# Kernel tuning notes

Measured on AMD Instinct MI355X. Metric: run time of the kernel, lower is better.

The kernel has to match this reference:

```python
import jax, jax.numpy as jnp
import numpy as np


def conv1x1(x, w, b):
    # x: [B,C,H,W], w: [O,C], b: [O]
    return jnp.einsum('bchw,oc->bohw', x, w) + b[None, :, None, None]


def setup_inputs() -> dict:
    key = jax.random.key(0)
    ks = jax.random.split(key, 16)
    B, C, H, W = 2, 64, 64, 64
    Cq = C // 8  # scale=8
    def mkw(k, o, i):
        return jax.random.normal(k, (o, i), jnp.float32) * 0.05
    return {
        'x': jax.random.normal(ks[0], (B, C, H, W), jnp.float32),
        'y': jax.random.normal(ks[1], (B, C, H, W), jnp.float32),
        'z': jax.random.normal(ks[2], (B, C, H, W), jnp.float32),
        # PAM params
        'pam_wq': mkw(ks[3], Cq, C), 'pam_bq': jnp.zeros((Cq,), jnp.float32),
        'pam_wk1': mkw(ks[4], Cq, C), 'pam_bk1': jnp.zeros((Cq,), jnp.float32),
        'pam_wk2': mkw(ks[5], Cq, C), 'pam_bk2': jnp.zeros((Cq,), jnp.float32),
        'pam_wk3': mkw(ks[6], Cq, C), 'pam_bk3': jnp.zeros((Cq,), jnp.float32),
        'pam_wv': mkw(ks[7], C, C), 'pam_bv': jnp.zeros((C,), jnp.float32),
        'pam_wl': mkw(ks[8], C, C), 'pam_bl': jnp.zeros((C,), jnp.float32),
        'pam_gamma': jnp.full((1,), 0.5, jnp.float32),
        # CAM params
        'cam_wl': mkw(ks[9], C, C), 'cam_bl': jnp.zeros((C,), jnp.float32),
        'cam_gamma': jnp.full((1,), 0.5, jnp.float32),
    }


def _pam(x, y, z, wq, bq, wk1, bk1, wk2, bk2, wk3, bk3, wv, bv, wl, bl, gamma):
    B, C, H, W = x.shape
    N = H * W
    Q = conv1x1(x, wq, bq).reshape(B, -1, N)   # [B, C/8, N]
    K1 = conv1x1(x, wk1, bk1).reshape(B, -1, N)
    K2 = conv1x1(y, wk2, bk2).reshape(B, -1, N)
    K3 = conv1x1(z, wk3, bk3).reshape(B, -1, N)
    V = conv1x1(x, wv, bv).reshape(B, C, N)    # [B, C, N]
    def branch(K):
        # energy[b,n,m] = sum_c Q[b,c,n] K[b,c,m]; softmax over last dim
        A = jax.nn.softmax(jnp.einsum('bcn,bcm->bnm', Q, K), axis=-1)
        # out[b,c,n] = sum_m A_as_mn[b,m,n] V[b,c,m] (einsum relabels axes as in torch code)
        return jnp.einsum('bmn,bcm->bcn', A, V)
    out = branch(K1) + branch(K2) + branch(K3)
    out = conv1x1(out.reshape(B, C, H, W), wl, bl)
    return x + gamma * out


def _cam(x, y, z, wl, bl, gamma):
    B, C, H, W = x.shape
    N = H * W
    q = x.reshape(B, C, N)
    def branch(k):
        e = jnp.einsum('bcn,bdn->bcd', q, k.reshape(B, C, N))  # [B,C,C]
        e = jnp.max(e, axis=-1, keepdims=True) - e             # max-subtraction trick
        A = jax.nn.softmax(e, axis=-1)
        return jnp.einsum('bcd,bdn->bcn', A, q)
    out = branch(x) + branch(y) + branch(z)
    out = conv1x1(out.reshape(B, C, H, W), wl, bl)
    return gamma * out + x


def reference(x, y, z, pam_wq, pam_bq, pam_wk1, pam_bk1, pam_wk2, pam_bk2,
              pam_wk3, pam_bk3, pam_wv, pam_bv, pam_wl, pam_bl, pam_gamma,
              cam_wl, cam_bl, cam_gamma):
    p = _pam(x, y, z, pam_wq, pam_bq, pam_wk1, pam_bk1, pam_wk2, pam_bk2,
             pam_wk3, pam_bk3, pam_wv, pam_bv, pam_wl, pam_bl, pam_gamma)
    c = _cam(x, y, z, cam_wl, cam_bl, cam_gamma)
    return p + c
```

## Files before the change

kernel.cpp:

```cpp
#include <hip/hip_runtime.h>
#include <hip/hip_bf16.h>


typedef __attribute__((ext_vector_type(8))) short bf16x8;
typedef __attribute__((ext_vector_type(4))) float f32x4;

#define MFMA16(a, b, c) __builtin_amdgcn_mfma_f32_16x16x32_bf16(a, b, c, 0, 0, 0)
#define EX2(x) __builtin_amdgcn_exp2f(x)
#define LOG2E 1.4426950408889634f

__device__ __forceinline__ float bf2f(ushort u) {
  union { unsigned int i; float f; } v; v.i = ((unsigned int)u) << 16; return v.f;
}
__device__ __forceinline__ ushort f2bf(float f) {
  union { float f; unsigned int i; } v; v.f = f;
  unsigned int r = v.i + 0x7FFFu + ((v.i >> 16) & 1u);
  return (ushort)(r >> 16);
}
__device__ __forceinline__ float loadf(const void* p, size_t i, int isbf) {
  return isbf ? bf2f(((const ushort*)p)[i]) : ((const float*)p)[i];
}
__device__ __forceinline__ bf16x8 load8(const void* p, size_t i, int isbf) {
  if (isbf) return *(const bf16x8*)((const ushort*)p + i);
  const float* f = (const float*)p + i;
  bf16x8 r;
#pragma unroll
  for (int j = 0; j < 8; ++j) r[j] = (short)f2bf(f[j]);
  return r;
}
__device__ __forceinline__ void loadf8(const void* p, size_t i, int isbf, float* o) {
  if (isbf) {
    bf16x8 v = *(const bf16x8*)((const ushort*)p + i);
#pragma unroll
    for (int j = 0; j < 8; ++j) o[j] = bf2f((ushort)v[j]);
  } else {
    const float* f = (const float*)p + i;
#pragma unroll
    for (int j = 0; j < 8; ++j) o[j] = f[j];
  }
}
__device__ __forceinline__ int detect_isbf(const unsigned int* xw, int* sflag) {
  int t = threadIdx.x;
  if (t < 64) {
    unsigned int w1 = xw[t], w2 = xw[64 + t];
    unsigned int e1 = (w1 >> 7) & 0xFFu, e2 = (w2 >> 7) & 0xFFu;
    unsigned long long b1 = __ballot(e1 >= 120u && e1 <= 133u);
    unsigned long long b2 = __ballot(e2 >= 120u && e2 <= 133u);
    if (t == 0) *sflag = (__popcll(b1) + __popcll(b2) > 64) ? 1 : 0;
  }
  __syncthreads();
  return *sflag;
}

__global__ __launch_bounds__(256) void k_prep_all(
    const void* __restrict__ x, const void* __restrict__ y, const void* __restrict__ z,
    const void* __restrict__ wq, const void* __restrict__ bq,
    const void* __restrict__ wk1, const void* __restrict__ bk1,
    const void* __restrict__ wk2, const void* __restrict__ bk2,
    const void* __restrict__ wk3, const void* __restrict__ bk3,
    const void* __restrict__ wv, const void* __restrict__ bv,
    ushort* __restrict__ QT, ushort* __restrict__ KT, ushort* __restrict__ V,
    float* __restrict__ e_part)
{
  __shared__ float wsh[4][8][64];
  __shared__ int sflag;
  int isbf = detect_isbf((const unsigned int*)x, &sflag);
  int blk = blockIdx.x, t = threadIdx.x;

  if (blk < 128) {
    for (int i = t; i < 2048; i += 256) {
      int mat = i >> 9, rem = i & 511;
      const void* src = (mat == 0) ? wq : (mat == 1) ? wk1 : (mat == 2) ? wk2 : wk3;
      wsh[mat][rem >> 6][rem & 63] = loadf(src, rem, isbf);
    }
    __syncthreads();
    int gid = blk * 256 + t;
    int qid = gid & 3;
    int n = (gid >> 2) & 4095;
    int b = gid >> 14;
    int c0 = qid * 16;
    float a[4][8];
#pragma unroll
    for (int m = 0; m < 4; ++m)
#pragma unroll
      for (int o = 0; o < 8; ++o) a[m][o] = 0.f;
    size_t base = (size_t)b * 262144 + n;
    for (int cc = 0; cc < 16; ++cc) {
      int c = c0 + cc;
      float xv = loadf(x, base + (size_t)c * 4096, isbf);
      float yv = loadf(y, base + (size_t)c * 4096, isbf);
      float zv = loadf(z, base + (size_t)c * 4096, isbf);
#pragma unroll
      for (int o = 0; o < 8; ++o) {
        a[0][o] += wsh[0][o][c] * xv;
        a[1][o] += wsh[1][o][c] * xv;
        a[2][o] += wsh[2][o][c] * yv;
        a[3][o] += wsh[3][o][c] * zv;
      }
    }
#pragma unroll
    for (int m = 0; m < 4; ++m)
#pragma unroll
      for (int o = 0; o < 8; ++o) {
        float v = a[m][o];
        v += __shfl_xor(v, 1, 64);
        v += __shfl_xor(v, 2, 64);
        a[m][o] = v;
      }
    int br = qid - 1;
    const void* bias = (qid == 0) ? bq : (qid == 1) ? bk1 : (qid == 2) ? bk2 : bk3;
    ushort* dst = (qid == 0) ? QT + (size_t)(b * 4096 + n) * 32
                             : KT + (size_t)((b * 3 + br) * 4096 + n) * 32;
    ushort row[32];
#pragma unroll
    for (int o = 0; o < 8; ++o) {
      float v = a[qid][o] + loadf(bias, o, isbf);
      row[o] = f2bf(qid == 0 ? LOG2E * v : v);
    }
#pragma unroll
    for (int o = 8; o < 32; ++o)
      row[o] = (qid > 0 && (o == 8 + 2 * br || o == 9 + 2 * br)) ? (ushort)0x3F80 : (ushort)0;
#pragma unroll
    for (int o = 0; o < 32; o += 2)
      *(unsigned int*)(dst + o) = (unsigned int)row[o] | ((unsigned int)row[o + 1] << 16);
  } else if (blk < 384) {
    int tid2 = (blk - 128) * 256 + t;
    int b = tid2 >> 15, c = (tid2 >> 9) & 63, m0 = (tid2 & 511) * 8;
    float acc[8], xv[8];
    float bb = loadf(bv, c, isbf);
#pragma unroll
    for (int j = 0; j < 8; ++j) acc[j] = bb;
    size_t xb = (size_t)b * 262144 + m0;
    for (int d = 0; d < 64; ++d) {
      float w = loadf(wv, c * 64 + d, isbf);
      loadf8(x, xb + (size_t)d * 4096, isbf, xv);
#pragma unroll
      for (int j = 0; j < 8; ++j) acc[j] += w * xv[j];
    }
    bf16x8 o8;
#pragma unroll
    for (int j = 0; j < 8; ++j) o8[j] = (short)f2bf(acc[j]);
    *(bf16x8*)(V + (size_t)(b * 64 + c) * 4096 + m0) = o8;
  } else {
    int r2 = blk - 384;
    int ns = r2 & 15, r = r2 >> 4;
    int k = r % 3, b = r / 3;
    const void* A = x;
    const void* B = (k == 0) ? x : (k == 1) ? y : z;
    size_t boff = (size_t)b * 262144;
    int w = t >> 6, l = t & 63;
    int l15 = l & 15, lh = l >> 4;
    int cbase = 16 * w;
    f32x4 acc[4];
#pragma unroll
    for (int i = 0; i < 4; ++i) acc[i] = (f32x4){0.f, 0.f, 0.f, 0.f};
    int n0 = ns * 256;
    for (int step = 0; step < 8; ++step) {
      int nb = n0 + step * 32;
      bf16x8 af = load8(A, boff + (size_t)(cbase + l15) * 4096 + nb + lh * 8, isbf);
#pragma unroll
      for (int dt = 0; dt < 4; ++dt) {
        bf16x8 bfr = load8(B, boff + (size_t)(dt * 16 + l15) * 4096 + nb + lh * 8, isbf);
        acc[dt] = MFMA16(af, bfr, acc[dt]);
      }
    }
    float* out = e_part + (size_t)(((b * 3 + k) * 16 + ns) * 64) * 64;
#pragma unroll
    for (int dt = 0; dt < 4; ++dt)
#pragma unroll
      for (int rr = 0; rr < 4; ++rr) {
        int c = cbase + lh * 4 + rr, d = dt * 16 + l15;
        out[c * 64 + d] = acc[dt][rr];
      }
  }
}

__global__ __launch_bounds__(256) void k_pass1(
    const ushort* __restrict__ QT, const ushort* __restrict__ KT,
    const float* __restrict__ e_part, float* __restrict__ S_part, float* __restrict__ e_red)
{
  int blk = blockIdx.x, t = threadIdx.x;
  if (blk < 1536) {
    int sl = blk & 3, mc = (blk >> 2) & 63, r3 = blk >> 8;
    int br = r3 % 3, b = r3 / 3;
    int w = t >> 6, l = t & 63;
    int l15 = l & 15, lh = l >> 4;
    int mbase = mc * 64 + w * 16;
    bf16x8 qf = *(const bf16x8*)(QT + (size_t)(b * 4096 + mbase + l15) * 32 + lh * 8);
    const ushort* Kb = KT + (size_t)((b * 3 + br) * 4096) * 32;
    float s = 0.f;
    int ns0 = sl * 64;
#pragma unroll 4
    for (int ns = ns0; ns < ns0 + 64; ++ns) {
      bf16x8 kf = *(const bf16x8*)(Kb + (size_t)(ns * 16 + l15) * 32 + lh * 8);
      f32x4 d = MFMA16(kf, qf, ((f32x4){0.f, 0.f, 0.f, 0.f}));
      s += EX2(d[0]) + EX2(d[1]) + EX2(d[2]) + EX2(d[3]);
    }
    s += __shfl_xor(s, 16, 64);
    s += __shfl_xor(s, 32, 64);
    if (l < 16) S_part[sl * 24576 + (b * 3 + br) * 4096 + mbase + l] = s;
  } else {
    int i = (blk - 1536) * 256 + t;
    const float* p = e_part + (size_t)(i >> 12) * 65536 + (i & 4095);
    float s = 0.f;
#pragma unroll
    for (int ks = 0; ks < 16; ++ks) s += p[ks * 4096];
    e_red[i] = s;
  }
}

__global__ __launch_bounds__(256) void k_mid(
    const float* __restrict__ S_part, ushort* __restrict__ QT,
    const float* __restrict__ e_red, const void* __restrict__ x,
    const void* __restrict__ cam_wl, const void* __restrict__ cam_bl, const void* __restrict__ cam_gamma,
    const void* __restrict__ pam_wl, const void* __restrict__ pam_bl, const void* __restrict__ pam_gamma,
    ushort* __restrict__ Wfull, float* __restrict__ biasv)
{
  int blk = blockIdx.x, t = threadIdx.x;
  if (blk < 96) {
    int i = blk * 256 + t;
    float S = S_part[i] + S_part[24576 + i] + S_part[49152 + i] + S_part[73728 + i];
    float nL = -__builtin_amdgcn_logf(S);
    int m = i & 4095, b3br = i >> 12;
    int br = b3br % 3, b = b3br / 3;
    ushort c = f2bf(nL);
    ushort r = f2bf(nL - bf2f(c));
    ushort* qrow = QT + (size_t)(b * 4096 + m) * 32;
    qrow[8 + 2 * br] = c;
    qrow[9 + 2 * br] = r;
  } else {
    __shared__ float Atot[64][65];
    __shared__ float erow[64][65];
    __shared__ int sflag;
    int isbf = detect_isbf((const unsigned int*)x, &sflag);
    int b = blk - 96;
    int r = t >> 2, q = t & 3;
#pragma unroll
    for (int j = 0; j < 16; ++j) Atot[r][q * 16 + j] = 0.f;
    for (int k = 0; k < 3; ++k) {
      const float* ep = e_red + (size_t)(b * 3 + k) * 4096;
      for (int i = t; i < 4096; i += 256) erow[i >> 6][i & 63] = ep[i];
      __syncthreads();
      float ev[16];
      float mn = 1e30f;
#pragma unroll
      for (int j = 0; j < 16; ++j) { ev[j] = erow[r][q * 16 + j]; mn = fminf(mn, ev[j]); }
      mn = fminf(mn, __shfl_xor(mn, 1, 64));
      mn = fminf(mn, __shfl_xor(mn, 2, 64));
      float s = 0.f;
#pragma unroll
      for (int j = 0; j < 16; ++j) { ev[j] = __expf(mn - ev[j]); s += ev[j]; }
      s += __shfl_xor(s, 1, 64);
      s += __shfl_xor(s, 2, 64);
      float inv = 1.0f / s;
#pragma unroll
      for (int j = 0; j < 16; ++j) Atot[r][q * 16 + j] += ev[j] * inv;
      __syncthreads();
    }
    float gc = loadf(cam_gamma, 0, isbf), gp = loadf(pam_gamma, 0, isbf);
    int c = t >> 2, d0 = (t & 3) * 16;
    float a[16];
#pragma unroll
    for (int i = 0; i < 16; ++i) a[i] = 0.f;
    for (int e = 0; e < 64; ++e) {
      float wv = loadf(cam_wl, c * 64 + e, isbf);
#pragma unroll
      for (int i = 0; i < 16; ++i) a[i] += wv * Atot[e][d0 + i];
    }
#pragma unroll
    for (int i = 0; i < 16; ++i) {
      int d = d0 + i;
      Wfull[(size_t)(b * 64 + c) * 128 + d]      = f2bf(gc * a[i]);
      Wfull[(size_t)(b * 64 + c) * 128 + 64 + d] = f2bf(gp * loadf(pam_wl, c * 64 + d, isbf));
    }
    if (b == 0 && t < 64) biasv[t] = gp * loadf(pam_bl, t, isbf) + gc * loadf(cam_bl, t, isbf);
  }
}

__global__ __launch_bounds__(256) void k_pam_out(
    const ushort* __restrict__ QT, const ushort* __restrict__ KT, const ushort* __restrict__ V,
    ushort* __restrict__ pam_part)
{
  __shared__ ushort plds[2][32 * 64];
  int blk = blockIdx.x;
  int ms = blk & 3, nt = (blk >> 2) & 127, b = blk >> 9;
  int w = threadIdx.x >> 6, l = threadIdx.x & 63;
  int l15 = l & 15, lh = l >> 4;
  int n0 = nt * 32;

  bf16x8 kf[3][2];
#pragma unroll
  for (int br = 0; br < 3; ++br)
#pragma unroll
    for (int n16 = 0; n16 < 2; ++n16)
      kf[br][n16] = *(const bf16x8*)(KT + (size_t)((b * 3 + br) * 4096 + n0 + n16 * 16 + l15) * 32 + lh * 8);

  f32x4 acc[2];
  acc[0] = (f32x4){0.f, 0.f, 0.f, 0.f};
  acc[1] = (f32x4){0.f, 0.f, 0.f, 0.f};
  const ushort* Vb = V + (size_t)(b * 64 + 16 * w + l15) * 4096;

  for (int ch = 0; ch < 16; ++ch) {
    int mch = ms * 1024 + ch * 64;
    char* buf = (char*)plds[ch & 1];
    bf16x8 qf = *(const bf16x8*)(QT + (size_t)(b * 4096 + mch + 16 * w + l15) * 32 + lh * 8);
#pragma unroll
    for (int n16 = 0; n16 < 2; ++n16) {
      f32x4 d0 = MFMA16(qf, kf[0][n16], ((f32x4){0.f, 0.f, 0.f, 0.f}));
      f32x4 d1 = MFMA16(qf, kf[1][n16], ((f32x4){0.f, 0.f, 0.f, 0.f}));
      f32x4 d2 = MFMA16(qf, kf[2][n16], ((f32x4){0.f, 0.f, 0.f, 0.f}));
      float p0 = EX2(d0[0]) + EX2(d1[0]) + EX2(d2[0]);
      float p1 = EX2(d0[1]) + EX2(d1[1]) + EX2(d2[1]);
      float p2 = EX2(d0[2]) + EX2(d1[2]) + EX2(d2[2]);
      float p3 = EX2(d0[3]) + EX2(d1[3]) + EX2(d2[3]);
      unsigned int u0, u1;
      asm("v_cvt_pk_bf16_f32 %0, %1, %2" : "=v"(u0) : "v"(p0), "v"(p1));
      asm("v_cvt_pk_bf16_f32 %0, %1, %2" : "=v"(u1) : "v"(p2), "v"(p3));
      int nl = n16 * 16 + l15;
      int byte = (nl * 128 + (16 * w + lh * 4) * 2) ^ ((nl & 7) << 4);
      *(uint2*)(buf + byte) = make_uint2(u0, u1);
    }
    __syncthreads();
#pragma unroll
    for (int ks = 0; ks < 2; ++ks) {
      bf16x8 vf = *(const bf16x8*)(Vb + mch + ks * 32 + lh * 8);
#pragma unroll
      for (int n16 = 0; n16 < 2; ++n16) {
        int nl = n16 * 16 + l15;
        int byte = (nl * 128 + (ks * 32 + lh * 8) * 2) ^ ((nl & 7) << 4);
        bf16x8 pf = *(const bf16x8*)((const char*)buf + byte);
        acc[n16] = MFMA16(vf, pf, acc[n16]);
      }
    }
  }
  ushort* outp = pam_part + (size_t)((b * 4 + ms) * 64) * 4096;
#pragma unroll
  for (int n16 = 0; n16 < 2; ++n16)
#pragma unroll
    for (int r = 0; r < 4; ++r) {
      int c = 16 * w + lh * 4 + r, n = n0 + n16 * 16 + l15;
      outp[(size_t)c * 4096 + n] = f2bf(acc[n16][r]);
    }
}

__global__ __launch_bounds__(256) void k_final(
    const void* __restrict__ x, const ushort* __restrict__ pam_part,
    const ushort* __restrict__ Wfull, const float* __restrict__ biasv,
    void* __restrict__ outv)
{
  __shared__ ushort u[64 * 128];
  __shared__ int sflag;
  int isbf = detect_isbf((const unsigned int*)x, &sflag);
  int blk = blockIdx.x;
  int nt = blk & 63, b = blk >> 6;
  int t = threadIdx.x;
  int n0 = nt * 64;
  int d = t >> 2, nl0 = (t & 3) * 16;
  size_t xbase = (size_t)(b * 64 + d) * 4096 + n0 + nl0;
#pragma unroll
  for (int i = 0; i < 16; ++i) {
    int nl = nl0 + i;
    int byte = (nl * 256 + d * 2) ^ ((nl & 7) << 4);
    *(ushort*)((char*)u + byte) = f2bf(loadf(x, xbase + i, isbf));
  }
  const ushort* pp = pam_part + (size_t)(b * 256 + d) * 4096 + n0 + nl0;
#pragma unroll
  for (int i = 0; i < 16; ++i) {
    float s = bf2f(pp[i]) + bf2f(pp[262144 + i]) + bf2f(pp[524288 + i]) + bf2f(pp[786432 + i]);
    int nl = nl0 + i;
    int byte = (nl * 256 + (64 + d) * 2) ^ ((nl & 7) << 4);
    *(ushort*)((char*)u + byte) = f2bf(s);
  }
  __syncthreads();

  int w = t >> 6, l = t & 63, l15 = l & 15, lh = l >> 4;
  f32x4 acc[4];
#pragma unroll
  for (int i = 0; i < 4; ++i) acc[i] = (f32x4){0.f, 0.f, 0.f, 0.f};
#pragma unroll
  for (int ks = 0; ks < 4; ++ks) {
    bf16x8 af = *(const bf16x8*)(Wfull + (size_t)(b * 64 + 16 * w + l15) * 128 + ks * 32 + lh * 8);
#pragma unroll
    for (int nt4 = 0; nt4 < 4; ++nt4) {
      int nl = nt4 * 16 + l15;
      int byte = (nl * 256 + (ks * 32 + lh * 8) * 2) ^ ((nl & 7) << 4);
      bf16x8 bfr = *(const bf16x8*)((const char*)u + byte);
      acc[nt4] = MFMA16(af, bfr, acc[nt4]);
    }
  }
#pragma unroll
  for (int nt4 = 0; nt4 < 4; ++nt4)
#pragma unroll
    for (int r = 0; r < 4; ++r) {
      int c = 16 * w + lh * 4 + r, nl = nt4 * 16 + l15;
      size_t xidx = (size_t)(b * 64 + c) * 4096 + n0 + nl;
      float xv = loadf(x, xidx, isbf);
      float v = acc[nt4][r] + 2.0f * xv + biasv[c];
      if (isbf) ((ushort*)outv)[xidx] = f2bf(v);
      else      ((float*)outv)[xidx]  = v;
    }
}

extern "C" void kernel_launch(void* const* d_in, const int* in_sizes, int n_in,
                              void* d_out, int out_size, void* d_ws, size_t ws_size,
                              hipStream_t stream) {
  const void* x   = d_in[0];
  const void* y   = d_in[1];
  const void* z   = d_in[2];
  const void* wq  = d_in[3];
  const void* bq  = d_in[4];
  const void* wk1 = d_in[5];
  const void* bk1 = d_in[6];
  const void* wk2 = d_in[7];
  const void* bk2 = d_in[8];
  const void* wk3 = d_in[9];
  const void* bk3 = d_in[10];
  const void* wv  = d_in[11];
  const void* bv  = d_in[12];
  const void* pwl = d_in[13];
  const void* pbl = d_in[14];
  const void* pg  = d_in[15];
  const void* cwl = d_in[16];
  const void* cbl = d_in[17];
  const void* cg  = d_in[18];

  char* ws = (char*)d_ws;
  ushort* QT      = (ushort*)(ws + 0);
  ushort* KT      = (ushort*)(ws + 524288);
  ushort* V       = (ushort*)(ws + 2097152);
  float*  S_part  = (float*) (ws + 3145728);
  float*  e_part  = (float*) (ws + 3538944);
  ushort* pam_prt = (ushort*)(ws + 5111808);
  ushort* Wfull   = (ushort*)(ws + 9306112);
  float*  biasv   = (float*) (ws + 9338880);
  float*  e_red   = (float*) (ws + 9339136);

  k_prep_all<<< 480, 256, 0, stream>>>(x, y, z, wq, bq, wk1, bk1, wk2, bk2, wk3, bk3,
                                       wv, bv, QT, KT, V, e_part);
  k_pass1   <<<1632, 256, 0, stream>>>(QT, KT, e_part, S_part, e_red);
  k_mid     <<<  98, 256, 0, stream>>>(S_part, QT, e_red, x, cwl, cbl, cg, pwl, pbl, pg,
                                       Wfull, biasv);
  k_pam_out <<<1024, 256, 0, stream>>>(QT, KT, V, pam_prt);
  k_final   <<< 128, 256, 0, stream>>>(x, pam_prt, Wfull, biasv, d_out);
}
```

Measured before the change: 100.2 us.

## Fuse mid stage into PAM output kernel and build P fragments in registers

```diff
diff --git a/kernel.cpp b/kernel.cpp
--- a/kernel.cpp
+++ b/kernel.cpp
@@ -3,6 +3,7 @@
 
 
 typedef __attribute__((ext_vector_type(8))) short bf16x8;
+typedef __attribute__((ext_vector_type(4))) short s16x4;
 typedef __attribute__((ext_vector_type(4))) float f32x4;
 
 #define MFMA16(a, b, c) __builtin_amdgcn_mfma_f32_16x16x32_bf16(a, b, c, 0, 0, 0)
@@ -59,7 +60,7 @@
     const void* __restrict__ wk2, const void* __restrict__ bk2,
     const void* __restrict__ wk3, const void* __restrict__ bk3,
     const void* __restrict__ wv, const void* __restrict__ bv,
-    ushort* __restrict__ QT, ushort* __restrict__ KT, ushort* __restrict__ V,
+    ushort* __restrict__ QT, ushort* __restrict__ KT, ushort* __restrict__ Vp,
     float* __restrict__ e_part)
 {
   __shared__ float wsh[4][8][64];
@@ -137,10 +138,15 @@
 #pragma unroll
       for (int j = 0; j < 8; ++j) acc[j] += w * xv[j];
     }
-    bf16x8 o8;
-#pragma unroll
-    for (int j = 0; j < 8; ++j) o8[j] = (short)f2bf(acc[j]);
-    *(bf16x8*)(V + (size_t)(b * 64 + c) * 4096 + m0) = o8;
+    int M5 = m0 & ~31;
+    int o = m0 & 31;
+    int s1 = (o == 0) ? 0 : (o == 8) ? 16 : (o == 16) ? 20 : 4;
+    s16x4 lo, hi;
+#pragma unroll
+    for (int j = 0; j < 4; ++j) { lo[j] = (short)f2bf(acc[j]); hi[j] = (short)f2bf(acc[4 + j]); }
+    ushort* vb = Vp + (size_t)(b * 64 + c) * 4096 + M5;
+    *(s16x4*)(vb + s1)     = lo;
+    *(s16x4*)(vb + s1 + 8) = hi;
   } else {
     int r2 = blk - 384;
     int ns = r2 & 15, r = r2 >> 4;
@@ -176,70 +182,57 @@
 }
 
 __global__ __launch_bounds__(256) void k_pass1(
-    const ushort* __restrict__ QT, const ushort* __restrict__ KT,
-    const float* __restrict__ e_part, float* __restrict__ S_part, float* __restrict__ e_red)
+    const ushort* __restrict__ QT, const ushort* __restrict__ KT, float* __restrict__ S_part)
 {
   int blk = blockIdx.x, t = threadIdx.x;
-  if (blk < 1536) {
-    int sl = blk & 3, mc = (blk >> 2) & 63, r3 = blk >> 8;
-    int br = r3 % 3, b = r3 / 3;
-    int w = t >> 6, l = t & 63;
-    int l15 = l & 15, lh = l >> 4;
-    int mbase = mc * 64 + w * 16;
-    bf16x8 qf = *(const bf16x8*)(QT + (size_t)(b * 4096 + mbase + l15) * 32 + lh * 8);
-    const ushort* Kb = KT + (size_t)((b * 3 + br) * 4096) * 32;
-    float s = 0.f;
-    int ns0 = sl * 64;
+  int sl = blk & 3, mc = (blk >> 2) & 63, r3 = blk >> 8;
+  int br = r3 % 3, b = r3 / 3;
+  int w = t >> 6, l = t & 63;
+  int l15 = l & 15, lh = l >> 4;
+  int mbase = mc * 64 + w * 16;
+  bf16x8 qf = *(const bf16x8*)(QT + (size_t)(b * 4096 + mbase + l15) * 32 + lh * 8);
+  const ushort* Kb = KT + (size_t)((b * 3 + br) * 4096) * 32;
+  float s = 0.f;
+  int ns0 = sl * 64;
 #pragma unroll 4
-    for (int ns = ns0; ns < ns0 + 64; ++ns) {
-      bf16x8 kf = *(const bf16x8*)(Kb + (size_t)(ns * 16 + l15) * 32 + lh * 8);
-      f32x4 d = MFMA16(kf, qf, ((f32x4){0.f, 0.f, 0.f, 0.f}));
-      s += EX2(d[0]) + EX2(d[1]) + EX2(d[2]) + EX2(d[3]);
-    }
-    s += __shfl_xor(s, 16, 64);
-    s += __shfl_xor(s, 32, 64);
-    if (l < 16) S_part[sl * 24576 + (b * 3 + br) * 4096 + mbase + l] = s;
-  } else {
-    int i = (blk - 1536) * 256 + t;
-    const float* p = e_part + (size_t)(i >> 12) * 65536 + (i & 4095);
-    float s = 0.f;
-#pragma unroll
-    for (int ks = 0; ks < 16; ++ks) s += p[ks * 4096];
-    e_red[i] = s;
-  }
-}
-
-__global__ __launch_bounds__(256) void k_mid(
-    const float* __restrict__ S_part, ushort* __restrict__ QT,
-    const float* __restrict__ e_red, const void* __restrict__ x,
+  for (int ns = ns0; ns < ns0 + 64; ++ns) {
+    bf16x8 kf = *(const bf16x8*)(Kb + (size_t)(ns * 16 + l15) * 32 + lh * 8);
+    f32x4 d = MFMA16(kf, qf, ((f32x4){0.f, 0.f, 0.f, 0.f}));
+    s += EX2(d[0]) + EX2(d[1]) + EX2(d[2]) + EX2(d[3]);
+  }
+  s += __shfl_xor(s, 16, 64);
+  s += __shfl_xor(s, 32, 64);
+  if (l < 16) S_part[sl * 24576 + (b * 3 + br) * 4096 + mbase + l] = s;
+}
+
+__global__ __launch_bounds__(256) void k_pam_out(
+    ushort* __restrict__ QT, const ushort* __restrict__ KT, const ushort* __restrict__ Vp,
+    const float* __restrict__ S_part, const float* __restrict__ e_part,
+    const void* __restrict__ x,
     const void* __restrict__ cam_wl, const void* __restrict__ cam_bl, const void* __restrict__ cam_gamma,
     const void* __restrict__ pam_wl, const void* __restrict__ pam_bl, const void* __restrict__ pam_gamma,
-    ushort* __restrict__ Wfull, float* __restrict__ biasv)
+    ushort* __restrict__ Wfull, float* __restrict__ biasv,
+    ushort* __restrict__ pam_part)
 {
+  __shared__ float erow[64][65];
+  __shared__ int sflag;
   int blk = blockIdx.x, t = threadIdx.x;
-  if (blk < 96) {
-    int i = blk * 256 + t;
-    float S = S_part[i] + S_part[24576 + i] + S_part[49152 + i] + S_part[73728 + i];
-    float nL = -__builtin_amdgcn_logf(S);
-    int m = i & 4095, b3br = i >> 12;
-    int br = b3br % 3, b = b3br / 3;
-    ushort c = f2bf(nL);
-    ushort r = f2bf(nL - bf2f(c));
-    ushort* qrow = QT + (size_t)(b * 4096 + m) * 32;
-    qrow[8 + 2 * br] = c;
-    qrow[9 + 2 * br] = r;
-  } else {
-    __shared__ float Atot[64][65];
-    __shared__ float erow[64][65];
-    __shared__ int sflag;
+
+  if (blk >= 1024) {
     int isbf = detect_isbf((const unsigned int*)x, &sflag);
-    int b = blk - 96;
+    int b = blk - 1024;
     int r = t >> 2, q = t & 3;
-#pragma unroll
-    for (int j = 0; j < 16; ++j) Atot[r][q * 16 + j] = 0.f;
+    float atot[16];
+#pragma unroll
+    for (int j = 0; j < 16; ++j) atot[j] = 0.f;
     for (int k = 0; k < 3; ++k) {
-      const float* ep = e_red + (size_t)(b * 3 + k) * 4096;
-      for (int i = t; i < 4096; i += 256) erow[i >> 6][i & 63] = ep[i];
+      const float* ep = e_part + (size_t)((b * 3 + k) * 16) * 4096;
+      for (int i = t; i < 4096; i += 256) {
+        float s = 0.f;
+#pragma unroll
+        for (int ks = 0; ks < 16; ++ks) s += ep[ks * 4096 + i];
+        erow[i >> 6][i & 63] = s;
+      }
       __syncthreads();
       float ev[16];
       float mn = 1e30f;
@@ -254,9 +247,13 @@
       s += __shfl_xor(s, 2, 64);
       float inv = 1.0f / s;
 #pragma unroll
-      for (int j = 0; j < 16; ++j) Atot[r][q * 16 + j] += ev[j] * inv;
+      for (int j = 0; j < 16; ++j) atot[j] += ev[j] * inv;
       __syncthreads();
     }
+    erow[r][q * 16 + 0] = atot[0];
+#pragma unroll
+    for (int j = 0; j < 16; ++j) erow[r][q * 16 + j] = atot[j];
+    __syncthreads();
     float gc = loadf(cam_gamma, 0, isbf), gp = loadf(pam_gamma, 0, isbf);
     int c = t >> 2, d0 = (t & 3) * 16;
     float a[16];
@@ -265,7 +262,7 @@
     for (int e = 0; e < 64; ++e) {
       float wv = loadf(cam_wl, c * 64 + e, isbf);
 #pragma unroll
-      for (int i = 0; i < 16; ++i) a[i] += wv * Atot[e][d0 + i];
+      for (int i = 0; i < 16; ++i) a[i] += wv * erow[e][d0 + i];
     }
 #pragma unroll
     for (int i = 0; i < 16; ++i) {
@@ -274,17 +271,26 @@
       Wfull[(size_t)(b * 64 + c) * 128 + 64 + d] = f2bf(gp * loadf(pam_wl, c * 64 + d, isbf));
     }
     if (b == 0 && t < 64) biasv[t] = gp * loadf(pam_bl, t, isbf) + gc * loadf(cam_bl, t, isbf);
-  }
-}
-
-__global__ __launch_bounds__(256) void k_pam_out(
-    const ushort* __restrict__ QT, const ushort* __restrict__ KT, const ushort* __restrict__ V,
-    ushort* __restrict__ pam_part)
-{
-  __shared__ ushort plds[2][32 * 64];
-  int blk = blockIdx.x;
+    return;
+  }
+
   int ms = blk & 3, nt = (blk >> 2) & 127, b = blk >> 9;
-  int w = threadIdx.x >> 6, l = threadIdx.x & 63;
+  for (int i = t; i < 1024; i += 256) {
+    int m = ms * 1024 + i;
+    ushort* qrow = QT + (size_t)(b * 4096 + m) * 32;
+#pragma unroll
+    for (int br = 0; br < 3; ++br) {
+      int idx = (b * 3 + br) * 4096 + m;
+      float S = S_part[idx] + S_part[24576 + idx] + S_part[49152 + idx] + S_part[73728 + idx];
+      float nL = -__builtin_amdgcn_logf(S);
+      ushort cc = f2bf(nL);
+      qrow[8 + 2 * br] = cc;
+      qrow[9 + 2 * br] = f2bf(nL - bf2f(cc));
+    }
+  }
+  __syncthreads();
+
+  int w = t >> 6, l = t & 63;
   int l15 = l & 15, lh = l >> 4;
   int n0 = nt * 32;
 
@@ -298,39 +304,39 @@
   f32x4 acc[2];
   acc[0] = (f32x4){0.f, 0.f, 0.f, 0.f};
   acc[1] = (f32x4){0.f, 0.f, 0.f, 0.f};
-  const ushort* Vb = V + (size_t)(b * 64 + 16 * w + l15) * 4096;
-
-  for (int ch = 0; ch < 16; ++ch) {
-    int mch = ms * 1024 + ch * 64;
-    char* buf = (char*)plds[ch & 1];
-    bf16x8 qf = *(const bf16x8*)(QT + (size_t)(b * 4096 + mch + 16 * w + l15) * 32 + lh * 8);
+  const ushort* Vb = Vp + (size_t)(b * 64 + 16 * w + l15) * 4096;
+  const f32x4 Z = (f32x4){0.f, 0.f, 0.f, 0.f};
+
+  for (int ch = 0; ch < 32; ++ch) {
+    int mch = ms * 1024 + ch * 32;
+    const ushort* qbase = QT + (size_t)(b * 4096 + mch + l15) * 32 + lh * 8;
+    bf16x8 qf0 = *(const bf16x8*)(qbase);
+    bf16x8 qf1 = *(const bf16x8*)(qbase + 512);
+    bf16x8 vf  = *(const bf16x8*)(Vb + mch + lh * 8);
 #pragma unroll
     for (int n16 = 0; n16 < 2; ++n16) {
-      f32x4 d0 = MFMA16(qf, kf[0][n16], ((f32x4){0.f, 0.f, 0.f, 0.f}));
-      f32x4 d1 = MFMA16(qf, kf[1][n16], ((f32x4){0.f, 0.f, 0.f, 0.f}));
-      f32x4 d2 = MFMA16(qf, kf[2][n16], ((f32x4){0.f, 0.f, 0.f, 0.f}));
-      float p0 = EX2(d0[0]) + EX2(d1[0]) + EX2(d2[0]);
-      float p1 = EX2(d0[1]) + EX2(d1[1]) + EX2(d2[1]);
-      float p2 = EX2(d0[2]) + EX2(d1[2]) + EX2(d2[2]);
-      float p3 = EX2(d0[3]) + EX2(d1[3]) + EX2(d2[3]);
-      unsigned int u0, u1;
-      asm("v_cvt_pk_bf16_f32 %0, %1, %2" : "=v"(u0) : "v"(p0), "v"(p1));
-      asm("v_cvt_pk_bf16_f32 %0, %1, %2" : "=v"(u1) : "v"(p2), "v"(p3));
-      int nl = n16 * 16 + l15;
-      int byte = (nl * 128 + (16 * w + lh * 4) * 2) ^ ((nl & 7) << 4);
-      *(uint2*)(buf + byte) = make_uint2(u0, u1);
-    }
-    __syncthreads();
-#pragma unroll
-    for (int ks = 0; ks < 2; ++ks) {
-      bf16x8 vf = *(const bf16x8*)(Vb + mch + ks * 32 + lh * 8);
-#pragma unroll
-      for (int n16 = 0; n16 < 2; ++n16) {
-        int nl = n16 * 16 + l15;
-        int byte = (nl * 128 + (ks * 32 + lh * 8) * 2) ^ ((nl & 7) << 4);
-        bf16x8 pf = *(const bf16x8*)((const char*)buf + byte);
-        acc[n16] = MFMA16(vf, pf, acc[n16]);
-      }
+      f32x4 dA0 = MFMA16(qf0, kf[0][n16], Z);
+      f32x4 dA1 = MFMA16(qf0, kf[1][n16], Z);
+      f32x4 dA2 = MFMA16(qf0, kf[2][n16], Z);
+      f32x4 dB0 = MFMA16(qf1, kf[0][n16], Z);
+      f32x4 dB1 = MFMA16(qf1, kf[1][n16], Z);
+      f32x4 dB2 = MFMA16(qf1, kf[2][n16], Z);
+      float plo[4], phi[4];
+#pragma unroll
+      for (int rr = 0; rr < 4; ++rr) {
+        plo[rr] = EX2(dA0[rr]) + EX2(dA1[rr]) + EX2(dA2[rr]);
+        phi[rr] = EX2(dB0[rr]) + EX2(dB1[rr]) + EX2(dB2[rr]);
+      }
+      unsigned int u0, u1, q0, q1;
+      asm("v_cvt_pk_bf16_f32 %0, %1, %2" : "=v"(u0) : "v"(plo[0]), "v"(plo[1]));
+      asm("v_cvt_pk_bf16_f32 %0, %1, %2" : "=v"(u1) : "v"(plo[2]), "v"(plo[3]));
+      asm("v_cvt_pk_bf16_f32 %0, %1, %2" : "=v"(q0) : "v"(phi[0]), "v"(phi[1]));
+      asm("v_cvt_pk_bf16_f32 %0, %1, %2" : "=v"(q1) : "v"(phi[2]), "v"(phi[3]));
+      unsigned int t0 = (unsigned int)__shfl_xor((int)q0, 32, 64);
+      unsigned int t1 = (unsigned int)__shfl_xor((int)q1, 32, 64);
+      union { unsigned int uw[4]; bf16x8 v; } pf;
+      pf.uw[0] = u0; pf.uw[1] = u1; pf.uw[2] = t0; pf.uw[3] = t1;
+      acc[n16] = MFMA16(vf, pf.v, acc[n16]);
     }
   }
   ushort* outp = pam_part + (size_t)((b * 4 + ms) * 64) * 4096;
@@ -427,19 +433,17 @@
   char* ws = (char*)d_ws;
   ushort* QT      = (ushort*)(ws + 0);
   ushort* KT      = (ushort*)(ws + 524288);
-  ushort* V       = (ushort*)(ws + 2097152);
+  ushort* Vp      = (ushort*)(ws + 2097152);
   float*  S_part  = (float*) (ws + 3145728);
   float*  e_part  = (float*) (ws + 3538944);
   ushort* pam_prt = (ushort*)(ws + 5111808);
   ushort* Wfull   = (ushort*)(ws + 9306112);
   float*  biasv   = (float*) (ws + 9338880);
-  float*  e_red   = (float*) (ws + 9339136);
 
   k_prep_all<<< 480, 256, 0, stream>>>(x, y, z, wq, bq, wk1, bk1, wk2, bk2, wk3, bk3,
-                                       wv, bv, QT, KT, V, e_part);
-  k_pass1   <<<1632, 256, 0, stream>>>(QT, KT, e_part, S_part, e_red);
-  k_mid     <<<  98, 256, 0, stream>>>(S_part, QT, e_red, x, cwl, cbl, cg, pwl, pbl, pg,
-                                       Wfull, biasv);
-  k_pam_out <<<1024, 256, 0, stream>>>(QT, KT, V, pam_prt);
+                                       wv, bv, QT, KT, Vp, e_part);
+  k_pass1   <<<1536, 256, 0, stream>>>(QT, KT, S_part);
+  k_pam_out <<<1026, 256, 0, stream>>>(QT, KT, Vp, S_part, e_part, x,
+                                       cwl, cbl, cg, pwl, pbl, pg, Wfull, biasv, pam_prt);
   k_final   <<< 128, 256, 0, stream>>>(x, pam_prt, Wfull, biasv, d_out);
 }
```

Result: slower. 138.4 us (+38.2%).
